# Kernel optimization log

Hardware: AMD Instinct MI355X
Metric: run time of the kernel (lower is better)

## Reference

```python
import jax, jax.numpy as jnp
import numpy as np

D_MODEL = 512
NUM_HEADS = 16
D_HEAD = D_MODEL // NUM_HEADS
B, L = 2, 2048


def setup_inputs() -> dict:
    key = jax.random.key(0)
    ks = jax.random.split(key, 16)
    s = 1.0 / np.sqrt(D_MODEL)
    return {
        "query": jax.random.normal(ks[0], (B, L, D_MODEL), jnp.float32),
        "key": jax.random.normal(ks[1], (B, L, D_MODEL), jnp.float32),
        "value": jax.random.normal(ks[2], (B, L, D_MODEL), jnp.float32),
        "pos_embedding": jax.random.normal(ks[3], (L, D_MODEL), jnp.float32),
        "Wq": jax.random.normal(ks[4], (D_MODEL, D_MODEL), jnp.float32) * s,
        "bq": jnp.zeros((D_MODEL,), jnp.float32),
        "Wk": jax.random.normal(ks[5], (D_MODEL, D_MODEL), jnp.float32) * s,
        "bk": jnp.zeros((D_MODEL,), jnp.float32),
        "Wv": jax.random.normal(ks[6], (D_MODEL, D_MODEL), jnp.float32) * s,
        "bv": jnp.zeros((D_MODEL,), jnp.float32),
        "Wp": jax.random.normal(ks[7], (D_MODEL, D_MODEL), jnp.float32) * s,
        "u_bias": jax.random.normal(ks[8], (NUM_HEADS, D_HEAD), jnp.float32) * 0.1,
        "v_bias": jax.random.normal(ks[9], (NUM_HEADS, D_HEAD), jnp.float32) * 0.1,
        "Wo": jax.random.normal(ks[10], (D_MODEL, D_MODEL), jnp.float32) * s,
        "bo": jnp.zeros((D_MODEL,), jnp.float32),
    }


def _relative_shift(pos_score):
    # pos_score: (B, H, L, L) -> Transformer-XL pad/view shift
    b, h, l1, l2 = pos_score.shape
    padded = jnp.pad(pos_score, ((0, 0), (0, 0), (0, 0), (1, 0)))  # (B,H,L,L+1)
    padded = padded.reshape(b, h, l2 + 1, l1)
    return padded[:, :, 1:].reshape(b, h, l1, l2)


def reference(query, key, value, pos_embedding, Wq, bq, Wk, bk, Wv, bv, Wp,
              u_bias, v_bias, Wo, bo):
    b = value.shape[0]
    scale = 1.0 / np.sqrt(D_MODEL)

    def split_heads(x):  # (B, L, D) -> (B, H, L, dh)
        return x.reshape(b, -1, NUM_HEADS, D_HEAD).transpose(0, 2, 1, 3)

    q = split_heads(query @ Wq.T + bq)
    k = split_heads(key @ Wk.T + bk)
    v = split_heads(value @ Wv.T + bv)
    p = (pos_embedding @ Wp.T).reshape(1, -1, NUM_HEADS, D_HEAD).transpose(0, 2, 1, 3)

    # content score: (q + u) K^T   (bias broadcast over queries)
    content_score = jnp.einsum('bhid,bhjd->bhij', q, k)
    content_score = content_score + jnp.einsum('hd,bhjd->bhj', u_bias, k)[:, :, None, :]

    # position score: (q + v) P^T, then relative shift
    pos_score = jnp.einsum('bhid,zhjd->bhij', q, p)
    pos_score = pos_score + jnp.einsum('hd,zhjd->zhj', v_bias, p)[:, :, None, :]
    pos_score = _relative_shift(pos_score)

    score = (content_score + pos_score) * scale
    attn = jax.nn.softmax(score, axis=-1)
    context = jnp.einsum('bhij,bhjd->bhid', attn, v)  # (B,H,L,dh)
    context = context.transpose(0, 2, 1, 3).reshape(b, -1, D_MODEL)
    return context @ Wo.T + bo
```

## Files before the change

kernel.cpp:

```cpp
#include <hip/hip_runtime.h>

typedef __attribute__((ext_vector_type(8))) short bf16x8;
typedef __attribute__((ext_vector_type(4))) float f32x4;
typedef __attribute__((ext_vector_type(2))) float f32x2;

#define MFMA16(a, b, c) __builtin_amdgcn_mfma_f32_16x16x32_bf16(a, b, c, 0, 0, 0)

__device__ __forceinline__ unsigned int cvtpk(float lo, float hi) {
  unsigned int r;
  asm("v_cvt_pk_bf16_f32 %0, %1, %2" : "=v"(r) : "v"(lo), "v"(hi));
  return r;
}
__device__ __forceinline__ float exp2fast(float x) {
  float r;
  asm("v_exp_f32 %0, %1" : "=v"(r) : "v"(x));
  return r;
}
__device__ __forceinline__ unsigned short f2bf(float f) {
  union { float f; unsigned int u; } x; x.f = f;
  unsigned int u = x.u;
  return (unsigned short)((u + 0x7FFFu + ((u >> 16) & 1u)) >> 16);
}
__device__ __forceinline__ bf16x8 mk8(unsigned int w0, unsigned int w1,
                                      unsigned int w2, unsigned int w3) {
  union { unsigned int w[4]; bf16x8 v; } u;
  u.w[0] = w0; u.w[1] = w1; u.w[2] = w2; u.w[3] = w3;
  return u.v;
}

#define CSCALE 0.0637669439631016f

__global__ __launch_bounds__(256) void proj_fused(
    const float* __restrict__ Xq, const float* __restrict__ Xk,
    const float* __restrict__ Xv, const float* __restrict__ Xp,
    const float* __restrict__ Wq, const float* __restrict__ Wk,
    const float* __restrict__ Wv, const float* __restrict__ Wp,
    const float* __restrict__ bq, const float* __restrict__ bk,
    const float* __restrict__ bv,
    const float* __restrict__ ub, const float* __restrict__ vb,
    unsigned short* __restrict__ QU, unsigned short* __restrict__ QV,
    unsigned short* __restrict__ Kb, unsigned short* __restrict__ Vs,
    unsigned short* __restrict__ Pb)
{
  const int mode = blockIdx.z;
  if (mode == 3 && blockIdx.x >= 16) return;
  const float* X = (mode == 0) ? Xq : (mode == 1) ? Xk : (mode == 2) ? Xv : Xp;
  const float* W = (mode == 0) ? Wq : (mode == 1) ? Wk : (mode == 2) ? Wv : Wp;
  const float* bias = (mode == 0) ? bq : (mode == 1) ? bk : (mode == 2) ? bv : nullptr;

  __shared__ __align__(16) unsigned short As[128][40];
  __shared__ __align__(16) unsigned short Bs[64][40];
  const int i0 = blockIdx.x * 128;
  const int o0 = blockIdx.y * 64;
  const int tid = threadIdx.x;
  const int w = tid >> 6, lane = tid & 63, g = lane >> 4, ln = lane & 15;

  f32x4 acc[2][4];
  #pragma unroll
  for (int rf = 0; rf < 2; ++rf)
    #pragma unroll
    for (int n = 0; n < 4; ++n) acc[rf][n] = (f32x4){0.f, 0.f, 0.f, 0.f};

  const int srow = tid >> 2;
  const int scol = (tid & 3) * 8;

  for (int k0 = 0; k0 < 512; k0 += 32) {
    if (k0) __syncthreads();
    {
      const float* sa = X + (size_t)(i0 + srow) * 512 + k0 + scol;
      f32x4 a0 = *(const f32x4*)sa;
      f32x4 a1 = *(const f32x4*)(sa + 4);
      uint4 av;
      av.x = cvtpk(a0[0], a0[1]); av.y = cvtpk(a0[2], a0[3]);
      av.z = cvtpk(a1[0], a1[1]); av.w = cvtpk(a1[2], a1[3]);
      *(uint4*)&As[srow][scol] = av;

      const float* sa2 = X + (size_t)(i0 + 64 + srow) * 512 + k0 + scol;
      f32x4 a2 = *(const f32x4*)sa2;
      f32x4 a3 = *(const f32x4*)(sa2 + 4);
      uint4 av2;
      av2.x = cvtpk(a2[0], a2[1]); av2.y = cvtpk(a2[2], a2[3]);
      av2.z = cvtpk(a3[0], a3[1]); av2.w = cvtpk(a3[2], a3[3]);
      *(uint4*)&As[64 + srow][scol] = av2;

      const float* sb = W + (size_t)(o0 + srow) * 512 + k0 + scol;
      f32x4 b0 = *(const f32x4*)sb;
      f32x4 b1 = *(const f32x4*)(sb + 4);
      uint4 bv2;
      bv2.x = cvtpk(b0[0], b0[1]); bv2.y = cvtpk(b0[2], b0[3]);
      bv2.z = cvtpk(b1[0], b1[1]); bv2.w = cvtpk(b1[2], b1[3]);
      *(uint4*)&Bs[srow][scol] = bv2;
    }
    __syncthreads();
    const bf16x8 af0 = *(const bf16x8*)&As[w * 32 + ln][g * 8];
    const bf16x8 af1 = *(const bf16x8*)&As[w * 32 + 16 + ln][g * 8];
    #pragma unroll
    for (int n = 0; n < 4; ++n) {
      const bf16x8 bfv = *(const bf16x8*)&Bs[n * 16 + ln][g * 8];
      acc[0][n] = MFMA16(af0, bfv, acc[0][n]);
      acc[1][n] = MFMA16(af1, bfv, acc[1][n]);
    }
  }

  #pragma unroll
  for (int rf = 0; rf < 2; ++rf) {
    #pragma unroll
    for (int n = 0; n < 4; ++n) {
      const int o = o0 + n * 16 + ln;
      const float bval = bias ? bias[o] : 0.f;
      const int h = o >> 5, d = o & 31;
      #pragma unroll
      for (int r = 0; r < 4; ++r) {
        const int i = i0 + w * 32 + rf * 16 + 4 * g + r;
        const float y = acc[rf][n][r] + bval;
        if (mode == 0) {
          const int b = i >> 11, li = i & 2047;
          const size_t a = (((size_t)(b * 16 + h)) * 2048 + li) * 32 + d;
          QU[a] = f2bf(CSCALE * (y + ub[o]));
          QV[a] = f2bf(CSCALE * (y + vb[o]));
        } else if (mode == 1) {
          const int b = i >> 11, li = i & 2047;
          const size_t a = (((size_t)(b * 16 + h)) * 2048 + li) * 32 + d;
          Kb[a] = f2bf(y);
        } else if (mode == 2) {
          const int b = i >> 11, li = i & 2047;
          const int blk = li >> 5, bb = li & 31;
          const int k = (bb < 16) ? (((bb >> 2) << 3) + (bb & 3))
                                  : ((((bb - 16) >> 2) << 3) + 4 + ((bb - 16) & 3));
          const size_t a = (((size_t)(b * 16 + h)) * 32 + d) * 2048 + (blk << 5) + k;
          Vs[a] = f2bf(y);
        } else {
          Pb[((size_t)h * 2048 + i) * 32 + d] = f2bf(y);
        }
      }
    }
  }
}

__global__ __launch_bounds__(256, 2) void attn_kernel(
    const unsigned short* __restrict__ QU, const unsigned short* __restrict__ QV,
    const unsigned short* __restrict__ Kb, const unsigned short* __restrict__ Vs,
    const unsigned short* __restrict__ Pb, unsigned short* __restrict__ CTX)
{
  __shared__ __align__(16) unsigned char U8[33 * 2084];
  __shared__ __align__(16) float sacc[4][16][32];
  __shared__ float slx[4][32];

  const int n = blockIdx.y * 64 + blockIdx.x;
  const int xcd = n & 7, slot = n >> 3;
  const int bh = (xcd << 2) | (slot >> 6);
  const int i0 = (slot & 63) * 32;
  const int h = bh & 15;
  const int b = bh >> 4;
  const int tid = threadIdx.x;
  const int w = tid >> 6, lane = tid & 63, g = lane >> 4, ln = lane & 15;

  const unsigned short* QUp = QU + (size_t)bh * 65536;
  const unsigned short* QVp = QV + (size_t)bh * 65536;
  const unsigned short* Kp  = Kb + (size_t)bh * 65536;
  const unsigned short* Vp  = Vs + (size_t)bh * 65536;
  const unsigned short* Pp  = Pb + (size_t)h * 65536;

  const f32x4 fz = (f32x4){0.f, 0.f, 0.f, 0.f};

  const bf16x8 quf0 = *(const bf16x8*)(QUp + (size_t)(i0 + ln) * 32 + g * 8);
  const bf16x8 quf1 = *(const bf16x8*)(QUp + (size_t)(i0 + 16 + ln) * 32 + g * 8);
  const bf16x8 qvf0 = *(const bf16x8*)(QVp + (size_t)(i0 + ln) * 32 + g * 8);
  const bf16x8 qvf1 = *(const bf16x8*)(QVp + (size_t)(i0 + 16 + ln) * 32 + g * 8);
  const int r32 = (i0 + 32 < 2048) ? (i0 + 32) : 2047;
  const bf16x8 qv32 = *(const bf16x8*)(QVp + (size_t)r32 * 32 + g * 8);

  if (tid < 32) U8[(tid + 1) * 2084 + (tid + 1)] = 0;

  const unsigned short* Pb0 = Pp + (size_t)(w * 16 + ln) * 32 + g * 8;
  bf16x8 pfb0 = *(const bf16x8*)(Pb0);
  bf16x8 pfb1 = *(const bf16x8*)(Pb0 + 64 * 32);
  bf16x8 pfb2 = *(const bf16x8*)(Pb0 + 128 * 32);
  bf16x8 pfb3 = *(const bf16x8*)(Pb0 + 192 * 32);
  const int wr0 = ln * 2084 + 4 * g + ln + 1;
  const int wr1 = (ln + 16) * 2084 + 4 * g + ln + 17;
  for (int itb = 0; itb < 8; ++itb) {
    #pragma unroll
    for (int k = 0; k < 4; ++k) {
      const int itt = itb * 4 + k;
      const int t0 = itt * 64 + w * 16;
      bf16x8 cur;
      if (k == 0) cur = pfb0; else if (k == 1) cur = pfb1;
      else if (k == 2) cur = pfb2; else cur = pfb3;
      if (itb < 7) {
        const bf16x8 nx = *(const bf16x8*)(Pb0 + (size_t)((itt + 4) * 64) * 32);
        if (k == 0) pfb0 = nx; else if (k == 1) pfb1 = nx;
        else if (k == 2) pfb2 = nx; else pfb3 = nx;
      }
      {
        f32x4 u0 = MFMA16(cur, qvf0, fz);
        unsigned int pk = __builtin_amdgcn_cvt_pk_fp8_f32(u0[0], u0[1], 0u, false);
        pk = __builtin_amdgcn_cvt_pk_fp8_f32(u0[2], u0[3], pk, true);
        unsigned char* wp = U8 + wr0 + t0;
        wp[0] = (unsigned char)(pk & 0xFFu);
        wp[1] = (unsigned char)((pk >> 8) & 0xFFu);
        wp[2] = (unsigned char)((pk >> 16) & 0xFFu);
        wp[3] = (unsigned char)(pk >> 24);
      }
      {
        f32x4 u1 = MFMA16(cur, qvf1, fz);
        unsigned int pk = __builtin_amdgcn_cvt_pk_fp8_f32(u1[0], u1[1], 0u, false);
        pk = __builtin_amdgcn_cvt_pk_fp8_f32(u1[2], u1[3], pk, true);
        unsigned char* wp = U8 + wr1 + t0;
        wp[0] = (unsigned char)(pk & 0xFFu);
        wp[1] = (unsigned char)((pk >> 8) & 0xFFu);
        wp[2] = (unsigned char)((pk >> 16) & 0xFFu);
        wp[3] = (unsigned char)(pk >> 24);
      }
      if (t0 <= 2014 - i0) {
        f32x4 u2 = MFMA16(cur, qv32, fz);
        if (ln == 0) {
          unsigned int qk = __builtin_amdgcn_cvt_pk_fp8_f32(u2[0], u2[1], 0u, false);
          qk = __builtin_amdgcn_cvt_pk_fp8_f32(u2[2], u2[3], qk, true);
          unsigned char* wq = U8 + 32 * 2084 + t0 + 4 * g + 33;
          wq[0] = (unsigned char)(qk & 0xFFu);
          wq[1] = (unsigned char)((qk >> 8) & 0xFFu);
          wq[2] = (unsigned char)((qk >> 16) & 0xFFu);
          wq[3] = (unsigned char)(qk >> 24);
        }
      }
    }
  }
  __syncthreads();

  f32x4 acc00 = fz, acc01 = fz, acc10 = fz, acc11 = fz;
  f32x4 accl0 = fz, accl1 = fz;
  const bf16x8 ones = mk8(0x3F803F80u, 0x3F803F80u, 0x3F803F80u, 0x3F803F80u);

  const unsigned short* kp = Kp + (size_t)(w * 512 + ln) * 32 + g * 8;
  bf16x8 kf[4];
  #pragma unroll
  for (int q = 0; q < 4; ++q) kf[q] = *(const bf16x8*)(kp + q * 512);

  const unsigned short* vpb = Vp + (size_t)ln * 2048 + w * 512 + 8 * g;
  bf16x8 vf00 = *(const bf16x8*)vpb;
  bf16x8 vf01 = *(const bf16x8*)(vpb + 32);
  bf16x8 vf10 = *(const bf16x8*)(vpb + 16 * 2048);
  bf16x8 vf11 = *(const bf16x8*)(vpb + 16 * 2048 + 32);

  for (int it = 0; it < 8; ++it) {
    const int jc = w * 512 + it * 64;
    const int jcg = jc + 4 * g;
    const int cb = jcg - i0;

    float pv0[16], pv1[16];
    if (jc > i0 + 31) {
      const unsigned char* b0 = U8 + (ln + 1) * 2084 + cb;
      const unsigned char* b1 = U8 + (ln + 17) * 2084 + cb;
      #pragma unroll
      for (int q = 0; q < 4; ++q) {
        const int d0 = *(const int*)(b0 + 16 * q);
        const f32x2 l0 = __builtin_amdgcn_cvt_pk_f32_fp8(d0, false);
        const f32x2 h0 = __builtin_amdgcn_cvt_pk_f32_fp8(d0, true);
        pv0[4 * q + 0] = l0[0]; pv0[4 * q + 1] = l0[1];
        pv0[4 * q + 2] = h0[0]; pv0[4 * q + 3] = h0[1];
        const int d1 = *(const int*)(b1 + 16 * q);
        const f32x2 l1 = __builtin_amdgcn_cvt_pk_f32_fp8(d1, false);
        const f32x2 h1 = __builtin_amdgcn_cvt_pk_f32_fp8(d1, true);
        pv1[4 * q + 0] = l1[0]; pv1[4 * q + 1] = l1[1];
        pv1[4 * q + 2] = h1[0]; pv1[4 * q + 3] = h1[1];
      }
    } else if (jc + 75 <= i0) {
      const unsigned char* a0 = U8 + ln * 2084 + cb + 2048;
      const unsigned char* a1 = U8 + (ln + 16) * 2084 + cb + 2048;
      #pragma unroll
      for (int q = 0; q < 4; ++q) {
        const int d0 = *(const int*)(a0 + 16 * q);
        const f32x2 l0 = __builtin_amdgcn_cvt_pk_f32_fp8(d0, false);
        const f32x2 h0 = __builtin_amdgcn_cvt_pk_f32_fp8(d0, true);
        pv0[4 * q + 0] = l0[0]; pv0[4 * q + 1] = l0[1];
        pv0[4 * q + 2] = h0[0]; pv0[4 * q + 3] = h0[1];
        const int d1 = *(const int*)(a1 + 16 * q);
        const f32x2 l1 = __builtin_amdgcn_cvt_pk_f32_fp8(d1, false);
        const f32x2 h1 = __builtin_amdgcn_cvt_pk_f32_fp8(d1, true);
        pv1[4 * q + 0] = l1[0]; pv1[4 * q + 1] = l1[1];
        pv1[4 * q + 2] = h1[0]; pv1[4 * q + 3] = h1[1];
      }
    } else {
      const int bA0 = ln * 2084 + cb + 2048;
      const int bB0 = (ln + 1) * 2084 + cb;
      const int bA1 = (ln + 16) * 2084 + cb + 2048;
      const int bB1 = (ln + 17) * 2084 + cb;
      const int djg0 = i0 + ln - jcg;
      const int djg1 = i0 + 16 + ln - jcg;
      #pragma unroll
      for (int e = 0; e < 16; ++e) {
        const int co = ((e >> 2) << 4) + (e & 3);
        const unsigned int b0 = U8[(co <= djg0 ? bA0 : bB0) + co];
        pv0[e] = __builtin_amdgcn_cvt_f32_fp8(b0, 0);
        const unsigned int b1 = U8[(co <= djg1 ? bA1 : bB1) + co];
        pv1[e] = __builtin_amdgcn_cvt_f32_fp8(b1, 0);
      }
    }

    f32x4 st0[4], st1[4];
    __builtin_amdgcn_s_setprio(1);
    #pragma unroll
    for (int q = 0; q < 4; ++q) {
      st0[q] = MFMA16(kf[q], quf0, fz);
      st1[q] = MFMA16(kf[q], quf1, fz);
    }
    __builtin_amdgcn_s_setprio(0);

    bf16x8 vn0, vn1, vn2, vn3;
    if (it < 7) {
      kp += 64 * 32;
      #pragma unroll
      for (int q = 0; q < 4; ++q) kf[q] = *(const bf16x8*)(kp + q * 512);
      const unsigned short* vp2 = vpb + 64;
      vn0 = *(const bf16x8*)vp2;
      vn1 = *(const bf16x8*)(vp2 + 32);
      vn2 = *(const bf16x8*)(vp2 + 16 * 2048);
      vn3 = *(const bf16x8*)(vp2 + 16 * 2048 + 32);
    }

    float p0[16], p1[16];
    #pragma unroll
    for (int e = 0; e < 16; ++e) {
      p0[e] = exp2fast(st0[e >> 2][e & 3] + pv0[e]);
      p1[e] = exp2fast(st1[e >> 2][e & 3] + pv1[e]);
    }

    const bf16x8 pfr00 = mk8(cvtpk(p0[0], p0[1]), cvtpk(p0[2], p0[3]),
                             cvtpk(p0[4], p0[5]), cvtpk(p0[6], p0[7]));
    const bf16x8 pfr01 = mk8(cvtpk(p0[8], p0[9]), cvtpk(p0[10], p0[11]),
                             cvtpk(p0[12], p0[13]), cvtpk(p0[14], p0[15]));
    const bf16x8 pfr10 = mk8(cvtpk(p1[0], p1[1]), cvtpk(p1[2], p1[3]),
                             cvtpk(p1[4], p1[5]), cvtpk(p1[6], p1[7]));
    const bf16x8 pfr11 = mk8(cvtpk(p1[8], p1[9]), cvtpk(p1[10], p1[11]),
                             cvtpk(p1[12], p1[13]), cvtpk(p1[14], p1[15]));

    __builtin_amdgcn_s_setprio(1);
    acc00 = MFMA16(vf00, pfr00, acc00);
    acc00 = MFMA16(vf01, pfr01, acc00);
    acc01 = MFMA16(vf10, pfr00, acc01);
    acc01 = MFMA16(vf11, pfr01, acc01);
    acc10 = MFMA16(vf00, pfr10, acc10);
    acc10 = MFMA16(vf01, pfr11, acc10);
    acc11 = MFMA16(vf10, pfr10, acc11);
    acc11 = MFMA16(vf11, pfr11, acc11);
    accl0 = MFMA16(ones, pfr00, accl0);
    accl0 = MFMA16(ones, pfr01, accl0);
    accl1 = MFMA16(ones, pfr10, accl1);
    accl1 = MFMA16(ones, pfr11, accl1);
    __builtin_amdgcn_s_setprio(0);

    if (it < 7) {
      vpb += 64;
      vf00 = vn0; vf01 = vn1; vf10 = vn2; vf11 = vn3;
    }
  }

  if (lane < 16) { slx[w][lane] = accl0[0]; slx[w][lane + 16] = accl1[0]; }
  #pragma unroll
  for (int r = 0; r < 4; ++r) {
    sacc[w][4 * g + r][ln] = acc00[r];
    sacc[w][4 * g + r][ln + 16] = acc10[r];
  }
  __syncthreads();

  for (int pp = tid; pp < 512; pp += 256) {
    const int d = pp >> 5, ii = pp & 31;
    const float Lt = (slx[0][ii] + slx[1][ii]) + (slx[2][ii] + slx[3][ii]);
    const float val = (sacc[0][d][ii] + sacc[1][d][ii]) +
                      (sacc[2][d][ii] + sacc[3][d][ii]);
    CTX[((size_t)(b * 2048 + i0 + ii)) * 512 + h * 32 + d] = f2bf(val / Lt);
  }
  __syncthreads();
  #pragma unroll
  for (int r = 0; r < 4; ++r) {
    sacc[w][4 * g + r][ln] = acc01[r];
    sacc[w][4 * g + r][ln + 16] = acc11[r];
  }
  __syncthreads();
  for (int pp = tid; pp < 512; pp += 256) {
    const int d = pp >> 5, ii = pp & 31;
    const float Lt = (slx[0][ii] + slx[1][ii]) + (slx[2][ii] + slx[3][ii]);
    const float val = (sacc[0][d][ii] + sacc[1][d][ii]) +
                      (sacc[2][d][ii] + sacc[3][d][ii]);
    CTX[((size_t)(b * 2048 + i0 + ii)) * 512 + h * 32 + 16 + d] = f2bf(val / Lt);
  }
}

__global__ __launch_bounds__(256) void out_gemm(
    const unsigned short* __restrict__ A, const float* __restrict__ W,
    const float* __restrict__ bias, float* __restrict__ out)
{
  __shared__ __align__(16) unsigned short As[128][40];
  __shared__ __align__(16) unsigned short Bs[64][40];
  const int i0 = blockIdx.x * 128;
  const int o0 = blockIdx.y * 64;
  const int tid = threadIdx.x;
  const int w = tid >> 6, lane = tid & 63, g = lane >> 4, ln = lane & 15;

  f32x4 acc[2][4];
  #pragma unroll
  for (int rf = 0; rf < 2; ++rf)
    #pragma unroll
    for (int n = 0; n < 4; ++n) acc[rf][n] = (f32x4){0.f, 0.f, 0.f, 0.f};

  const int srow = tid >> 2;
  const int scol = (tid & 3) * 8;

  for (int k0 = 0; k0 < 512; k0 += 32) {
    if (k0) __syncthreads();
    *(bf16x8*)&As[srow][scol] =
        *(const bf16x8*)(A + (size_t)(i0 + srow) * 512 + k0 + scol);
    *(bf16x8*)&As[64 + srow][scol] =
        *(const bf16x8*)(A + (size_t)(i0 + 64 + srow) * 512 + k0 + scol);
    {
      const float* sb = W + (size_t)(o0 + srow) * 512 + k0 + scol;
      f32x4 b0 = *(const f32x4*)sb;
      f32x4 b1 = *(const f32x4*)(sb + 4);
      uint4 bv2;
      bv2.x = cvtpk(b0[0], b0[1]); bv2.y = cvtpk(b0[2], b0[3]);
      bv2.z = cvtpk(b1[0], b1[1]); bv2.w = cvtpk(b1[2], b1[3]);
      *(uint4*)&Bs[srow][scol] = bv2;
    }
    __syncthreads();
    const bf16x8 af0 = *(const bf16x8*)&As[w * 32 + ln][g * 8];
    const bf16x8 af1 = *(const bf16x8*)&As[w * 32 + 16 + ln][g * 8];
    #pragma unroll
    for (int n = 0; n < 4; ++n) {
      const bf16x8 bfv = *(const bf16x8*)&Bs[n * 16 + ln][g * 8];
      acc[0][n] = MFMA16(af0, bfv, acc[0][n]);
      acc[1][n] = MFMA16(af1, bfv, acc[1][n]);
    }
  }

  #pragma unroll
  for (int rf = 0; rf < 2; ++rf) {
    #pragma unroll
    for (int n = 0; n < 4; ++n) {
      const int o = o0 + n * 16 + ln;
      const float bval = bias[o];
      #pragma unroll
      for (int r = 0; r < 4; ++r) {
        const int i = i0 + w * 32 + rf * 16 + 4 * g + r;
        out[(size_t)i * 512 + o] = acc[rf][n][r] + bval;
      }
    }
  }
}

extern "C" void kernel_launch(void* const* d_in, const int* in_sizes, int n_in,
                              void* d_out, int out_size, void* d_ws, size_t ws_size,
                              hipStream_t stream) {
  const float* query = (const float*)d_in[0];
  const float* key_  = (const float*)d_in[1];
  const float* value = (const float*)d_in[2];
  const float* pos   = (const float*)d_in[3];
  const float* Wq = (const float*)d_in[4];
  const float* bq = (const float*)d_in[5];
  const float* Wk = (const float*)d_in[6];
  const float* bk = (const float*)d_in[7];
  const float* Wv = (const float*)d_in[8];
  const float* bv = (const float*)d_in[9];
  const float* Wp = (const float*)d_in[10];
  const float* ub = (const float*)d_in[11];
  const float* vbias = (const float*)d_in[12];
  const float* Wo = (const float*)d_in[13];
  const float* bo = (const float*)d_in[14];

  char* ws = (char*)d_ws;
  unsigned short* QU  = (unsigned short*)(ws);
  unsigned short* QV  = (unsigned short*)(ws + 4194304);
  unsigned short* Kb  = (unsigned short*)(ws + 2 * 4194304);
  unsigned short* Vs  = (unsigned short*)(ws + 3 * 4194304);
  unsigned short* Pb  = (unsigned short*)(ws + 4 * 4194304);
  unsigned short* CTX = (unsigned short*)(ws + 4 * 4194304 + 2097152);

  proj_fused<<<dim3(32, 8, 4), dim3(256), 0, stream>>>(
      query, key_, value, pos, Wq, Wk, Wv, Wp, bq, bk, bv, ub, vbias,
      QU, QV, Kb, Vs, Pb);
  attn_kernel<<<dim3(64, 32), dim3(256), 0, stream>>>(QU, QV, Kb, Vs, Pb, CTX);
  out_gemm<<<dim3(32, 8), dim3(256), 0, stream>>>(CTX, Wo, bo, (float*)d_out);
}
```

Before: 135.4 us.

## Software-pipeline attention loop: prefetch next score MFMAs and position bias

Restructures the key-block loop into a software pipeline. The position-bias bytes and the QK^T MFMAs for block it+1 are issued during iteration it, so the exp/PV work of the current block overlaps the next block's memory loads and score computation. The loop is fully unrolled, and the V fragment loads move to the end of each iteration. This raises register pressure (extra st/pv buffers held across iterations), which could reduce occupancy or cause spills.

```diff
diff --git a/kernel.cpp b/kernel.cpp
--- a/kernel.cpp
+++ b/kernel.cpp
@@ -243,12 +243,11 @@
   bf16x8 vf10 = *(const bf16x8*)(vpb + 16 * 2048);
   bf16x8 vf11 = *(const bf16x8*)(vpb + 16 * 2048 + 32);
 
-  for (int it = 0; it < 8; ++it) {
-    const int jc = w * 512 + it * 64;
+  float pv0[16], pv1[16];
+  {
+    const int jc = w * 512;
     const int jcg = jc + 4 * g;
     const int cb = jcg - i0;
-
-    float pv0[16], pv1[16];
     if (jc > i0 + 31) {
       const unsigned char* b0 = U8 + (ln + 1) * 2084 + cb;
       const unsigned char* b1 = U8 + (ln + 17) * 2084 + cb;
@@ -297,26 +296,78 @@
         pv1[e] = __builtin_amdgcn_cvt_f32_fp8(b1, 0);
       }
     }
-
-    f32x4 st0[4], st1[4];
-    __builtin_amdgcn_s_setprio(1);
-    #pragma unroll
-    for (int q = 0; q < 4; ++q) {
-      st0[q] = MFMA16(kf[q], quf0, fz);
-      st1[q] = MFMA16(kf[q], quf1, fz);
-    }
-    __builtin_amdgcn_s_setprio(0);
-
-    bf16x8 vn0, vn1, vn2, vn3;
+  }
+  f32x4 st0[4], st1[4];
+  __builtin_amdgcn_s_setprio(1);
+  #pragma unroll
+  for (int q = 0; q < 4; ++q) {
+    st0[q] = MFMA16(kf[q], quf0, fz);
+    st1[q] = MFMA16(kf[q], quf1, fz);
+  }
+  __builtin_amdgcn_s_setprio(0);
+  kp += 64 * 32;
+  #pragma unroll
+  for (int q = 0; q < 4; ++q) kf[q] = *(const bf16x8*)(kp + q * 512);
+
+  #pragma unroll
+  for (int it = 0; it < 8; ++it) {
+    int raw0[4], raw1[4];
+    bool useraw = false;
+    float npv0[16], npv1[16];
     if (it < 7) {
-      kp += 64 * 32;
-      #pragma unroll
-      for (int q = 0; q < 4; ++q) kf[q] = *(const bf16x8*)(kp + q * 512);
-      const unsigned short* vp2 = vpb + 64;
-      vn0 = *(const bf16x8*)vp2;
-      vn1 = *(const bf16x8*)(vp2 + 32);
-      vn2 = *(const bf16x8*)(vp2 + 16 * 2048);
-      vn3 = *(const bf16x8*)(vp2 + 16 * 2048 + 32);
+      const int jc2 = w * 512 + (it + 1) * 64;
+      const int jcg2 = jc2 + 4 * g;
+      const int cb2 = jcg2 - i0;
+      if (jc2 > i0 + 31) {
+        const unsigned char* b0 = U8 + (ln + 1) * 2084 + cb2;
+        const unsigned char* b1 = U8 + (ln + 17) * 2084 + cb2;
+        #pragma unroll
+        for (int q = 0; q < 4; ++q) {
+          raw0[q] = *(const int*)(b0 + 16 * q);
+          raw1[q] = *(const int*)(b1 + 16 * q);
+        }
+        useraw = true;
+      } else if (jc2 + 75 <= i0) {
+        const unsigned char* a0 = U8 + ln * 2084 + cb2 + 2048;
+        const unsigned char* a1 = U8 + (ln + 16) * 2084 + cb2 + 2048;
+        #pragma unroll
+        for (int q = 0; q < 4; ++q) {
+          raw0[q] = *(const int*)(a0 + 16 * q);
+          raw1[q] = *(const int*)(a1 + 16 * q);
+        }
+        useraw = true;
+      } else {
+        const int bA0 = ln * 2084 + cb2 + 2048;
+        const int bB0 = (ln + 1) * 2084 + cb2;
+        const int bA1 = (ln + 16) * 2084 + cb2 + 2048;
+        const int bB1 = (ln + 17) * 2084 + cb2;
+        const int djg0 = i0 + ln - jcg2;
+        const int djg1 = i0 + 16 + ln - jcg2;
+        #pragma unroll
+        for (int e = 0; e < 16; ++e) {
+          const int co = ((e >> 2) << 4) + (e & 3);
+          const unsigned int b0v = U8[(co <= djg0 ? bA0 : bB0) + co];
+          npv0[e] = __builtin_amdgcn_cvt_f32_fp8(b0v, 0);
+          const unsigned int b1v = U8[(co <= djg1 ? bA1 : bB1) + co];
+          npv1[e] = __builtin_amdgcn_cvt_f32_fp8(b1v, 0);
+        }
+      }
+    }
+
+    f32x4 nst0[4], nst1[4];
+    if (it < 7) {
+      __builtin_amdgcn_s_setprio(1);
+      #pragma unroll
+      for (int q = 0; q < 4; ++q) {
+        nst0[q] = MFMA16(kf[q], quf0, fz);
+        nst1[q] = MFMA16(kf[q], quf1, fz);
+      }
+      __builtin_amdgcn_s_setprio(0);
+      if (it < 6) {
+        kp += 64 * 32;
+        #pragma unroll
+        for (int q = 0; q < 4; ++q) kf[q] = *(const bf16x8*)(kp + q * 512);
+      }
     }
 
     float p0[16], p1[16];
@@ -325,7 +376,6 @@
       p0[e] = exp2fast(st0[e >> 2][e & 3] + pv0[e]);
       p1[e] = exp2fast(st1[e >> 2][e & 3] + pv1[e]);
     }
-
     const bf16x8 pfr00 = mk8(cvtpk(p0[0], p0[1]), cvtpk(p0[2], p0[3]),
                              cvtpk(p0[4], p0[5]), cvtpk(p0[6], p0[7]));
     const bf16x8 pfr01 = mk8(cvtpk(p0[8], p0[9]), cvtpk(p0[10], p0[11]),
@@ -349,10 +399,32 @@
     accl1 = MFMA16(ones, pfr10, accl1);
     accl1 = MFMA16(ones, pfr11, accl1);
     __builtin_amdgcn_s_setprio(0);
-
     if (it < 7) {
       vpb += 64;
-      vf00 = vn0; vf01 = vn1; vf10 = vn2; vf11 = vn3;
+      vf00 = *(const bf16x8*)vpb;
+      vf01 = *(const bf16x8*)(vpb + 32);
+      vf10 = *(const bf16x8*)(vpb + 16 * 2048);
+      vf11 = *(const bf16x8*)(vpb + 16 * 2048 + 32);
+    }
+
+    if (it < 7) {
+      if (useraw) {
+        #pragma unroll
+        for (int q = 0; q < 4; ++q) {
+          const f32x2 l0 = __builtin_amdgcn_cvt_pk_f32_fp8(raw0[q], false);
+          const f32x2 h0 = __builtin_amdgcn_cvt_pk_f32_fp8(raw0[q], true);
+          npv0[4 * q + 0] = l0[0]; npv0[4 * q + 1] = l0[1];
+          npv0[4 * q + 2] = h0[0]; npv0[4 * q + 3] = h0[1];
+          const f32x2 l1 = __builtin_amdgcn_cvt_pk_f32_fp8(raw1[q], false);
+          const f32x2 h1 = __builtin_amdgcn_cvt_pk_f32_fp8(raw1[q], true);
+          npv1[4 * q + 0] = l1[0]; npv1[4 * q + 1] = l1[1];
+          npv1[4 * q + 2] = h1[0]; npv1[4 * q + 3] = h1[1];
+        }
+      }
+      #pragma unroll
+      for (int q = 0; q < 4; ++q) { st0[q] = nst0[q]; st1[q] = nst1[q]; }
+      #pragma unroll
+      for (int e = 0; e < 16; ++e) { pv0[e] = npv0[e]; pv1[e] = npv1[e]; }
     }
   }
 
```

Measured after the change: 131.0 us. -3.2%, faster.
